# Kernel optimization log

Measured on AMD Instinct MI355X. Metric: run time of the kernel, lower is better.

Reference implementation:

```python
import jax, jax.numpy as jnp
import numpy as np

VOCAB = 1024
CTX = 8
D = VOCAB * CTX  # flattened one-hot dim = Linear in/out features
BATCH = 1024


def setup_inputs() -> dict:
    key = jax.random.key(0)
    k1, k2, k3 = jax.random.split(key, 3)
    x = jax.random.randint(k1, (BATCH, CTX), 0, VOCAB)
    # nn.Linear params: weight (out, in) = (D, D), bias (D,)
    W = jax.random.normal(k2, (D, D), dtype=jnp.float32) * 0.02
    b = jax.random.normal(k3, (D,), dtype=jnp.float32) * 0.02
    return {"x": x, "W": W, "b": b}


def reference(x, W, b):
    B, T = x.shape
    # one_hot(x).view(B, T*V) @ W.T + b  ==  sum_t W[:, t*V + x[:,t]] + b
    flat_idx = jnp.arange(T) * VOCAB + x  # [B, T], values in [0, D)
    # gather weight columns: [D, B, T], sum over context positions -> [D, B]
    gathered = jnp.take(W, flat_idx, axis=1)
    logits_flat = gathered.sum(axis=-1).T + b  # [B, D]
    return logits_flat.reshape(B, T, VOCAB)
```

## Files before the change

kernel.cpp:

```cpp
#include <hip/hip_runtime.h>

#define VOCAB 1024
#define CTX 8
#define DDIM 8192
#define BATCH 1024
#define RDIM 16

__global__ __launch_bounds__(1024, 8) void fused_gather(
    const int* __restrict__ x, const float* __restrict__ W,
    const float* __restrict__ b, float* __restrict__ out) {
    __shared__ __align__(16) float lds[2][DDIM];
    const int tid = threadIdx.x;
    const int d0  = blockIdx.x * RDIM;

#define STAGE(BUF, DD)                                                         \
    {                                                                          \
        const float* _src = W + (size_t)(d0 + (DD)) * DDIM + tid * 4;          \
        __builtin_amdgcn_global_load_lds(                                      \
            (const __attribute__((address_space(1))) void*)(_src),             \
            (__attribute__((address_space(3))) void*)(&lds[(BUF)][tid * 4]),   \
            16, 0, 0);                                                         \
        __builtin_amdgcn_global_load_lds(                                      \
            (const __attribute__((address_space(1))) void*)(_src + 4096),      \
            (__attribute__((address_space(3))) void*)(&lds[(BUF)][4096 + tid * 4]), \
            16, 0, 0);                                                         \
    }

    STAGE(0, 0)

    const int4 xa = *reinterpret_cast<const int4*>(x + tid * CTX);
    const int4 xb = *reinterpret_cast<const int4*>(x + tid * CTX + 4);
    const int o0 = xa.x;
    const int o1 = 1 * VOCAB + xa.y;
    const int o2 = 2 * VOCAB + xa.z;
    const int o3 = 3 * VOCAB + xa.w;
    const int o4 = 4 * VOCAB + xb.x;
    const int o5 = 5 * VOCAB + xb.y;
    const int o6 = 6 * VOCAB + xb.z;
    const int o7 = 7 * VOCAB + xb.w;

    float acc[RDIM];

#pragma unroll
    for (int dl = 0; dl < RDIM; ++dl) {
        if (dl < RDIM - 1) {
            STAGE((dl + 1) & 1, dl + 1)
            asm volatile("s_waitcnt vmcnt(2)" ::: "memory");
        } else {
            asm volatile("s_waitcnt vmcnt(0)" ::: "memory");
        }
        __builtin_amdgcn_s_barrier();

        const float* buf = &lds[dl & 1][0];
        const float v0 = buf[o0];
        const float v1 = buf[o1];
        const float v2 = buf[o2];
        const float v3 = buf[o3];
        const float v4 = buf[o4];
        const float v5 = buf[o5];
        const float v6 = buf[o6];
        const float v7 = buf[o7];
        acc[dl] = ((v0 + v1) + (v2 + v3)) + ((v4 + v5) + (v6 + v7));

        if (dl < RDIM - 1)
            __builtin_amdgcn_s_barrier();
    }
#undef STAGE

    const float4 bv0 = *reinterpret_cast<const float4*>(b + d0);
    const float4 bv1 = *reinterpret_cast<const float4*>(b + d0 + 4);
    const float4 bv2 = *reinterpret_cast<const float4*>(b + d0 + 8);
    const float4 bv3 = *reinterpret_cast<const float4*>(b + d0 + 12);
    float* orow = out + (size_t)tid * DDIM + d0;
    float4 r;
    r.x = acc[0] + bv0.x;  r.y = acc[1] + bv0.y;
    r.z = acc[2] + bv0.z;  r.w = acc[3] + bv0.w;
    reinterpret_cast<float4*>(orow)[0] = r;
    r.x = acc[4] + bv1.x;  r.y = acc[5] + bv1.y;
    r.z = acc[6] + bv1.z;  r.w = acc[7] + bv1.w;
    reinterpret_cast<float4*>(orow)[1] = r;
    r.x = acc[8] + bv2.x;  r.y = acc[9] + bv2.y;
    r.z = acc[10] + bv2.z; r.w = acc[11] + bv2.w;
    reinterpret_cast<float4*>(orow)[2] = r;
    r.x = acc[12] + bv3.x; r.y = acc[13] + bv3.y;
    r.z = acc[14] + bv3.z; r.w = acc[15] + bv3.w;
    reinterpret_cast<float4*>(orow)[3] = r;
}

extern "C" void kernel_launch(void* const* d_in, const int* in_sizes, int n_in,
                              void* d_out, int out_size, void* d_ws, size_t ws_size,
                              hipStream_t stream) {
    const int*   x = (const int*)d_in[0];
    const float* W = (const float*)d_in[1];
    const float* b = (const float*)d_in[2];
    float*     out = (float*)d_out;

    hipLaunchKernelGGL(fused_gather, dim3(DDIM / RDIM), dim3(1024), 0, stream,
                       x, W, b, out);
}
```

Before: 441.0 us.

## Transpose output tile through LDS for coalesced stores and swizzle block order

The accumulated 1024x16 output tile is staged through a padded LDS arena (stride 17) so each wave writes contiguous 64-byte row segments instead of one 64-byte segment per thread spread across rows. Block indices are remapped so consecutive blocks handle strided output-column groups, which changes how concurrently running blocks map to W rows and output columns. The LDS arena is shared between the double buffer and the transpose buffer. It adds an extra barrier per iteration and an extra LDS round trip at the end.

After: 435.2 us. Within noise of the previous version (-1.3%).

```diff
diff --git a/kernel.cpp b/kernel.cpp
--- a/kernel.cpp
+++ b/kernel.cpp
@@ -5,31 +5,38 @@
 #define DDIM 8192
 #define BATCH 1024
 #define RDIM 16
+#define TSTR 17
+#define ARENA_FLOATS (BATCH * TSTR)
 
 __global__ __launch_bounds__(1024, 8) void fused_gather(
     const int* __restrict__ x, const float* __restrict__ W,
     const float* __restrict__ b, float* __restrict__ out) {
-    __shared__ __align__(16) float lds[2][DDIM];
+    __shared__ __align__(16) float arena[ARENA_FLOATS];
+    float* lds0 = arena;
+    float* lds1 = arena + DDIM;
+    float* tr   = arena;
+
     const int tid = threadIdx.x;
-    const int d0  = blockIdx.x * RDIM;
+    const int db = ((blockIdx.x & 7) << 6) + (blockIdx.x >> 3);
+    const int d0 = db * RDIM;
 
-#define STAGE(BUF, DD)                                                         \
+#define STAGE(DST, DD)                                                         \
     {                                                                          \
         const float* _src = W + (size_t)(d0 + (DD)) * DDIM + tid * 4;          \
         __builtin_amdgcn_global_load_lds(                                      \
             (const __attribute__((address_space(1))) void*)(_src),             \
-            (__attribute__((address_space(3))) void*)(&lds[(BUF)][tid * 4]),   \
+            (__attribute__((address_space(3))) void*)((DST) + tid * 4),        \
             16, 0, 0);                                                         \
         __builtin_amdgcn_global_load_lds(                                      \
             (const __attribute__((address_space(1))) void*)(_src + 4096),      \
-            (__attribute__((address_space(3))) void*)(&lds[(BUF)][4096 + tid * 4]), \
+            (__attribute__((address_space(3))) void*)((DST) + 4096 + tid * 4), \
             16, 0, 0);                                                         \
     }
 
-    STAGE(0, 0)
-
     const int4 xa = *reinterpret_cast<const int4*>(x + tid * CTX);
     const int4 xb = *reinterpret_cast<const int4*>(x + tid * CTX + 4);
+    STAGE(lds0, 0)
+
     const int o0 = xa.x;
     const int o1 = 1 * VOCAB + xa.y;
     const int o2 = 2 * VOCAB + xa.z;
@@ -43,15 +50,15 @@
 
 #pragma unroll
     for (int dl = 0; dl < RDIM; ++dl) {
+        const float* buf = (dl & 1) ? lds1 : lds0;
         if (dl < RDIM - 1) {
-            STAGE((dl + 1) & 1, dl + 1)
+            STAGE((dl & 1) ? lds0 : lds1, dl + 1)
             asm volatile("s_waitcnt vmcnt(2)" ::: "memory");
         } else {
             asm volatile("s_waitcnt vmcnt(0)" ::: "memory");
         }
         __builtin_amdgcn_s_barrier();
 
-        const float* buf = &lds[dl & 1][0];
         const float v0 = buf[o0];
         const float v1 = buf[o1];
         const float v2 = buf[o2];
@@ -62,29 +69,32 @@
         const float v7 = buf[o7];
         acc[dl] = ((v0 + v1) + (v2 + v3)) + ((v4 + v5) + (v6 + v7));
 
-        if (dl < RDIM - 1)
-            __builtin_amdgcn_s_barrier();
+        asm volatile("s_waitcnt lgkmcnt(0)" ::: "memory");
+        __builtin_amdgcn_s_barrier();
     }
 #undef STAGE
 
-    const float4 bv0 = *reinterpret_cast<const float4*>(b + d0);
-    const float4 bv1 = *reinterpret_cast<const float4*>(b + d0 + 4);
-    const float4 bv2 = *reinterpret_cast<const float4*>(b + d0 + 8);
-    const float4 bv3 = *reinterpret_cast<const float4*>(b + d0 + 12);
-    float* orow = out + (size_t)tid * DDIM + d0;
-    float4 r;
-    r.x = acc[0] + bv0.x;  r.y = acc[1] + bv0.y;
-    r.z = acc[2] + bv0.z;  r.w = acc[3] + bv0.w;
-    reinterpret_cast<float4*>(orow)[0] = r;
-    r.x = acc[4] + bv1.x;  r.y = acc[5] + bv1.y;
-    r.z = acc[6] + bv1.z;  r.w = acc[7] + bv1.w;
-    reinterpret_cast<float4*>(orow)[1] = r;
-    r.x = acc[8] + bv2.x;  r.y = acc[9] + bv2.y;
-    r.z = acc[10] + bv2.z; r.w = acc[11] + bv2.w;
-    reinterpret_cast<float4*>(orow)[2] = r;
-    r.x = acc[12] + bv3.x; r.y = acc[13] + bv3.y;
-    r.z = acc[14] + bv3.z; r.w = acc[15] + bv3.w;
-    reinterpret_cast<float4*>(orow)[3] = r;
+    float bv[RDIM];
+#pragma unroll
+    for (int k = 0; k < RDIM; ++k) bv[k] = b[d0 + k];
+
+#pragma unroll
+    for (int k = 0; k < RDIM; ++k) tr[tid * TSTR + k] = acc[k] + bv[k];
+    asm volatile("s_waitcnt lgkmcnt(0)" ::: "memory");
+    __builtin_amdgcn_s_barrier();
+
+    const int lane = tid & 63;
+    const int wid  = tid >> 6;
+    const int colg = (lane & 3) << 2;
+    const int rsub = lane >> 2;
+#pragma unroll
+    for (int c = 0; c < 4; ++c) {
+        const int row = (wid << 6) + (c << 4) + rsub;
+        const float* s = tr + row * TSTR + colg;
+        float4 v;
+        v.x = s[0]; v.y = s[1]; v.z = s[2]; v.w = s[3];
+        *reinterpret_cast<float4*>(out + (size_t)row * DDIM + d0 + colg) = v;
+    }
 }
 
 extern "C" void kernel_launch(void* const* d_in, const int* in_sizes, int n_in,
```
